# Kernel optimization log

Hardware: AMD Instinct MI355X
Metric: run time of the kernel (lower is better)

## Reference

```python
import jax, jax.numpy as jnp
import numpy as np

N = 50000
E = 800000
NFEAT = 256
NHID = 64
HEADS = 4
NCLASS = 16
NEG_SLOPE = 0.2


def setup_inputs() -> dict:
    key = jax.random.key(0)
    ks = jax.random.split(key, 12)
    g = lambda k, s, scale: (jax.random.normal(k, s, dtype=jnp.float32) * scale)
    inp = {
        "x": g(ks[0], (N, NFEAT), 1.0),
        "src": jax.random.randint(ks[1], (E,), 0, N, dtype=jnp.int32),
        "dst": jax.random.randint(ks[2], (E,), 0, N, dtype=jnp.int32),
        # layer 1 params (DGL GATConv: fc no-bias, attn_l/attn_r, output bias)
        "W1": g(ks[3], (NFEAT, HEADS * NHID), (2.0 / NFEAT) ** 0.5),
        "al1": g(ks[4], (HEADS, NHID), 0.1),
        "ar1": g(ks[5], (HEADS, NHID), 0.1),
        "b1": jnp.zeros((HEADS * NHID,), dtype=jnp.float32),
        # layer 2 params (1 head)
        "W2": g(ks[6], (HEADS * NHID, NCLASS), (2.0 / (HEADS * NHID)) ** 0.5),
        "al2": g(ks[7], (1, NCLASS), 0.1),
        "ar2": g(ks[8], (1, NCLASS), 0.1),
        "b2": jnp.zeros((NCLASS,), dtype=jnp.float32),
    }
    return inp


def gat_conv(x, src, dst, W, al, ar, b, heads, dh):
    # x: [N, Fin] -> feat: [N, H, D]
    n = x.shape[0]
    feat = (x @ W).reshape(n, heads, dh)
    el = jnp.einsum("nhd,hd->nh", feat, al)  # [N, H]
    er = jnp.einsum("nhd,hd->nh", feat, ar)
    e = jax.nn.leaky_relu(el[src] + er[dst], NEG_SLOPE)  # [E, H]
    # segment softmax over destination nodes
    emax = jax.ops.segment_max(e, dst, num_segments=n)
    emax = jnp.where(jnp.isfinite(emax), emax, jnp.float32(0.0))
    ex = jnp.exp(e - emax[dst])  # [E, H]
    denom = jax.ops.segment_sum(ex, dst, num_segments=n)  # [N, H]
    alpha = ex / denom[dst]  # [E, H]
    # gather src feats, weight, scatter-add to dst
    msg = feat[src] * alpha[:, :, None]  # [E, H, D]
    out = jax.ops.segment_sum(msg, dst, num_segments=n)  # [N, H, D]
    return out + b.reshape(1, heads, dh)


def reference(x, src, dst, W1, al1, ar1, b1, W2, al2, ar2, b2):
    h = gat_conv(x, src, dst, W1, al1, ar1, b1, HEADS, NHID)  # [N, 4, nhid]
    h = h.reshape(N, HEADS * NHID)
    h = jax.nn.elu(h)
    h = gat_conv(h, src, dst, W2, al2, ar2, b2, 1, NCLASS)  # [N, 1, nclass]
    h = h.reshape(N, NCLASS)
    return jax.nn.log_softmax(h, axis=1)
```

## Files before the change

kernel.cpp:

```cpp
#include <hip/hip_runtime.h>
#include <hip/hip_bf16.h>

#define N_NODES 50000
#define NP1     50001
#define N_EDGES 800000
#define NFEAT   256
#define NHID    64
#define HEADS   4
#define NCLASS  16
#define NEG_SLOPE 0.2f

#define NBLK  782
#define NBUCK 196
#define NSCAN (NBUCK * NBLK)
#define NSCB  150
#define MAXB  5120
#define NGB   391

typedef __attribute__((ext_vector_type(8))) short short8;
typedef __attribute__((ext_vector_type(4))) float floatx4;
typedef __attribute__((ext_vector_type(2))) float floatx2;

__device__ __forceinline__ float blo(unsigned int u) { return __uint_as_float(u << 16); }
__device__ __forceinline__ float bhi(unsigned int u) { return __uint_as_float(u & 0xffff0000u); }
__device__ __forceinline__ float b2f(unsigned short u) {
    return __uint_as_float(((unsigned int)u) << 16);
}
__device__ __forceinline__ unsigned short f2b(float f) {
    unsigned int x = __float_as_uint(f);
    unsigned int r = x + 0x7fffu + ((x >> 16) & 1u);
    return (unsigned short)(r >> 16);
}
__device__ __forceinline__ unsigned int pack2(float a, float b) {
    return (unsigned int)f2b(a) | ((unsigned int)f2b(b) << 16);
}
__device__ __forceinline__ float leaky(float x) { return fmaxf(x, NEG_SLOPE * x); }

__device__ __forceinline__ void fp8acc2(uint4 u, floatx2 exv, floatx2* acc) {
    acc[0] = __builtin_elementwise_fma(__builtin_amdgcn_cvt_pk_f32_fp8(u.x, 0), exv, acc[0]);
    acc[1] = __builtin_elementwise_fma(__builtin_amdgcn_cvt_pk_f32_fp8(u.x, 1), exv, acc[1]);
    acc[2] = __builtin_elementwise_fma(__builtin_amdgcn_cvt_pk_f32_fp8(u.y, 0), exv, acc[2]);
    acc[3] = __builtin_elementwise_fma(__builtin_amdgcn_cvt_pk_f32_fp8(u.y, 1), exv, acc[3]);
    acc[4] = __builtin_elementwise_fma(__builtin_amdgcn_cvt_pk_f32_fp8(u.z, 0), exv, acc[4]);
    acc[5] = __builtin_elementwise_fma(__builtin_amdgcn_cvt_pk_f32_fp8(u.z, 1), exv, acc[5]);
    acc[6] = __builtin_elementwise_fma(__builtin_amdgcn_cvt_pk_f32_fp8(u.w, 0), exv, acc[6]);
    acc[7] = __builtin_elementwise_fma(__builtin_amdgcn_cvt_pk_f32_fp8(u.w, 1), exv, acc[7]);
}

__global__ __launch_bounds__(256) void p1_kernel(
        const int* __restrict__ dst, int* __restrict__ bhist,
        const float* __restrict__ W1, const float* __restrict__ W2,
        const float* __restrict__ al1, const float* __restrict__ ar1,
        unsigned short* __restrict__ W1E, unsigned short* __restrict__ W2T) {
    __shared__ float tile[64][65];
    __shared__ int hist[NBUCK];
    int b = blockIdx.x, t = threadIdx.x;
    if (b < NBLK) {
        if (t < NBUCK) hist[t] = 0;
        __syncthreads();
        int e = (b * 256 + t) * 4;
        if (e < N_EDGES) {
            int4 d = *(const int4*)&dst[e];
            atomicAdd(&hist[d.x >> 8], 1);
            atomicAdd(&hist[d.y >> 8], 1);
            atomicAdd(&hist[d.z >> 8], 1);
            atomicAdd(&hist[d.w >> 8], 1);
        }
        __syncthreads();
        if (t < NBUCK) bhist[t * NBLK + b] = hist[t];
        return;
    }
    int pb = b - NBLK;
    if (pb < 16) {
        int tk = (pb & 3) * 64, tn = (pb >> 2) * 64;
        int tx = t & 63, ty = t >> 6;
#pragma unroll
        for (int r = 0; r < 16; ++r) {
            int row = ty * 16 + r;
            tile[row][tx] = W1[(tk + row) * 256 + tn + tx];
        }
        __syncthreads();
#pragma unroll
        for (int r = 0; r < 16; ++r) {
            int row = ty * 16 + r;
            W1E[(tn + row) * 256 + tk + tx] = f2b(tile[tx][row]);
        }
    } else if (pb < 20) {
        int h = pb - 16;
        int w = t >> 6, lane = t & 63;
        float alv = al1[h * 64 + lane];
        float arv = ar1[h * 64 + lane];
        for (int k = w; k < 256; k += 4) {
            float wv = W1[k * 256 + h * 64 + lane];
            float sl = wv * alv, sr = wv * arv;
#pragma unroll
            for (int off = 1; off < 64; off <<= 1) {
                sl += __shfl_xor(sl, off);
                sr += __shfl_xor(sr, off);
            }
            if (lane == 0) {
                W1E[(256 + h) * 256 + k] = f2b(sl);
                W1E[(260 + h) * 256 + k] = f2b(sr);
            }
        }
    } else {
        int n = t >> 4, k0 = (t & 15) * 16;
#pragma unroll
        for (int j = 0; j < 16; ++j)
            W2T[n * 256 + k0 + j] = f2b(W2[(k0 + j) * 16 + n]);
#pragma unroll
        for (int j = 0; j < 8; ++j)
            W1E[264 * 256 + j * 256 + t] = 0;
    }
}

__global__ __launch_bounds__(256) void scanA_kernel(const int* __restrict__ bhist,
                                                    int* __restrict__ partial,
                                                    int* __restrict__ bsum) {
    __shared__ int wsum[4];
    int t = threadIdx.x;
    int base = blockIdx.x * 1024 + t * 4;
    int v0 = (base + 0 < NSCAN) ? bhist[base + 0] : 0;
    int v1 = (base + 1 < NSCAN) ? bhist[base + 1] : 0;
    int v2 = (base + 2 < NSCAN) ? bhist[base + 2] : 0;
    int v3 = (base + 3 < NSCAN) ? bhist[base + 3] : 0;
    int s = v0 + v1 + v2 + v3;
    int lane = t & 63, w = t >> 6;
    int incl = s;
#pragma unroll
    for (int off = 1; off < 64; off <<= 1) {
        int x = __shfl_up(incl, off);
        if (lane >= off) incl += x;
    }
    if (lane == 63) wsum[w] = incl;
    __syncthreads();
    int woff = 0;
    for (int k = 0; k < w; ++k) woff += wsum[k];
    int excl = woff + incl - s;
    if (base + 0 < NSCAN) partial[base + 0] = excl;
    if (base + 1 < NSCAN) partial[base + 1] = excl + v0;
    if (base + 2 < NSCAN) partial[base + 2] = excl + v0 + v1;
    if (base + 3 < NSCAN) partial[base + 3] = excl + v0 + v1 + v2;
    if (t == 255) bsum[blockIdx.x] = woff + incl;
}

__global__ __launch_bounds__(256, 2) void p2g1_kernel(
        const int* __restrict__ src, const int* __restrict__ dst,
        const int* __restrict__ partial, const int* __restrict__ bsum,
        unsigned int* __restrict__ ebuf,
        const float* __restrict__ X, const unsigned short* __restrict__ BT,
        unsigned char* __restrict__ C, float* __restrict__ el, float* __restrict__ er) {
    __shared__ __align__(16) unsigned short As[128 * 40];
    __shared__ __align__(16) unsigned short Bs[272 * 40];
    __shared__ int wsum[4];
    __shared__ int sb[256];
    __shared__ int bs[NBUCK];
    __shared__ int lcnt[256];
    __shared__ int lofs[256];
    __shared__ int lfill[256];
    __shared__ unsigned int sorted[1024];

    int t = threadIdx.x;
    if (blockIdx.x >= NGB) {
        int b = blockIdx.x - NGB;
        int lane = t & 63, w = t >> 6;
        {
            int v = (t < NSCB) ? bsum[t] : 0;
            int incl = v;
#pragma unroll
            for (int off = 1; off < 64; off <<= 1) {
                int x = __shfl_up(incl, off);
                if (lane >= off) incl += x;
            }
            if (lane == 63) wsum[w] = incl;
            __syncthreads();
            int woff = 0;
            for (int k = 0; k < w; ++k) woff += wsum[k];
            sb[t] = woff + incl - v;
        }
        lcnt[t] = 0;
        __syncthreads();
        if (t < NBUCK) {
            int idx = t * NBLK + b;
            bs[t] = partial[idx] + sb[idx >> 10];
        }
        int e = (b * 256 + t) * 4;
        int4 d, s;
        bool valid = e < N_EDGES;
        if (valid) {
            d = *(const int4*)&dst[e];
            s = *(const int4*)&src[e];
            atomicAdd(&lcnt[d.x >> 8], 1);
            atomicAdd(&lcnt[d.y >> 8], 1);
            atomicAdd(&lcnt[d.z >> 8], 1);
            atomicAdd(&lcnt[d.w >> 8], 1);
        }
        __syncthreads();
        {
            int v = lcnt[t];
            int incl = v;
#pragma unroll
            for (int off = 1; off < 64; off <<= 1) {
                int x = __shfl_up(incl, off);
                if (lane >= off) incl += x;
            }
            if (lane == 63) wsum[w] = incl;
            __syncthreads();
            int woff = 0;
            for (int k = 0; k < w; ++k) woff += wsum[k];
            int excl = woff + incl - v;
            lofs[t] = excl;
            lfill[t] = excl;
        }
        __syncthreads();
        if (valid) {
            int p0 = atomicAdd(&lfill[d.x >> 8], 1);
            sorted[p0] = ((unsigned int)s.x << 16) | (unsigned int)d.x;
            int p1 = atomicAdd(&lfill[d.y >> 8], 1);
            sorted[p1] = ((unsigned int)s.y << 16) | (unsigned int)d.y;
            int p2 = atomicAdd(&lfill[d.z >> 8], 1);
            sorted[p2] = ((unsigned int)s.z << 16) | (unsigned int)d.z;
            int p3 = atomicAdd(&lfill[d.w >> 8], 1);
            sorted[p3] = ((unsigned int)s.w << 16) | (unsigned int)d.w;
        }
        __syncthreads();
        int ve = min(1024, N_EDGES - b * 1024);
        for (int i = t; i < ve; i += 256) {
            unsigned int p = sorted[i];
            int k = (p & 0xFFFFu) >> 8;
            ebuf[bs[k] + (i - lofs[k])] = p;
        }
        return;
    }

    int m0 = blockIdx.x * 128;
    int lane = t & 63, wm = t >> 6;
    int quad = lane >> 4, l16 = lane & 15;

    floatx4 acc[2][17];
#pragma unroll
    for (int i = 0; i < 2; ++i)
#pragma unroll
        for (int j = 0; j < 17; ++j) acc[i][j] = (floatx4){0.f, 0.f, 0.f, 0.f};

    int arow = t >> 1, ak = (t & 1) * 16;
    int grow = m0 + arow;
    const float* xrow = X + (size_t)grow * 256 + ak;

    for (int k0 = 0; k0 < 256; k0 += 32) {
        float4 v0 = make_float4(0.f, 0.f, 0.f, 0.f), v1 = v0, v2 = v0, v3 = v0;
        if (grow < N_NODES) {
            v0 = *(const float4*)(xrow + k0 + 0);
            v1 = *(const float4*)(xrow + k0 + 4);
            v2 = *(const float4*)(xrow + k0 + 8);
            v3 = *(const float4*)(xrow + k0 + 12);
        }
        uint4 p0, p1;
        p0.x = pack2(v0.x, v0.y); p0.y = pack2(v0.z, v0.w);
        p0.z = pack2(v1.x, v1.y); p0.w = pack2(v1.z, v1.w);
        p1.x = pack2(v2.x, v2.y); p1.y = pack2(v2.z, v2.w);
        p1.z = pack2(v3.x, v3.y); p1.w = pack2(v3.z, v3.w);
        *(uint4*)&As[arow * 40 + ak] = p0;
        *(uint4*)&As[arow * 40 + ak + 8] = p1;
#pragma unroll
        for (int i = 0; i < 5; ++i) {
            int ch = t + i * 256;
            if (ch < 1088) {
                int row = ch >> 2, off = (ch & 3) * 8;
                *(uint4*)&Bs[row * 40 + off] = *(const uint4*)(BT + row * 256 + k0 + off);
            }
        }
        __syncthreads();

        short8 a0 = *(const short8*)&As[(wm * 32 + l16) * 40 + quad * 8];
        short8 a1 = *(const short8*)&As[(wm * 32 + 16 + l16) * 40 + quad * 8];
#pragma unroll
        for (int nf = 0; nf < 17; ++nf) {
            short8 bb = *(const short8*)&Bs[(nf * 16 + l16) * 40 + quad * 8];
            acc[0][nf] = __builtin_amdgcn_mfma_f32_16x16x32_bf16(a0, bb, acc[0][nf], 0, 0, 0);
            acc[1][nf] = __builtin_amdgcn_mfma_f32_16x16x32_bf16(a1, bb, acc[1][nf], 0, 0, 0);
        }
        __syncthreads();
    }

#pragma unroll
    for (int mf = 0; mf < 2; ++mf) {
#pragma unroll
        for (int r = 0; r < 4; ++r) {
            int row = m0 + wm * 32 + mf * 16 + quad * 4 + r;
            if (row < N_NODES && l16 < 8) {
                float v = acc[mf][16][r];
                if (l16 < 4) el[row * 4 + l16] = v;
                else er[row * 4 + (l16 - 4)] = v;
            }
        }
    }

    unsigned short* scr = Bs + wm * 1536;
    int half = lane >> 5, l32 = lane & 31;
    int rrow = l32 >> 1, coff = (l32 & 1) * 8;
#pragma unroll
    for (int mf = 0; mf < 2; ++mf) {
#pragma unroll
        for (int p = 0; p < 8; ++p) {
            unsigned short* base = scr + (p & 1) * 768;
#pragma unroll
            for (int fr = 0; fr < 2; ++fr) {
                int nf = 2 * p + fr;
                unsigned short* fb = base + fr * 384;
#pragma unroll
                for (int r = 0; r < 4; ++r)
                    fb[(quad * 4 + r) * 24 + l16] = f2b(acc[mf][nf][r]);
            }
            uint4 val = *(const uint4*)(base + half * 384 + rrow * 24 + coff);
            int row = m0 + wm * 32 + mf * 16 + rrow;
            int nf = 2 * p + half;
            if (row < N_NODES) {
                float f0 = blo(val.x), f1 = bhi(val.x), f2 = blo(val.y), f3 = bhi(val.y);
                float f4 = blo(val.z), f5 = bhi(val.z), f6 = blo(val.w), f7 = bhi(val.w);
                int lo = __builtin_amdgcn_cvt_pk_fp8_f32(f0, f1, 0, 0);
                lo = __builtin_amdgcn_cvt_pk_fp8_f32(f2, f3, lo, 1);
                int hi = __builtin_amdgcn_cvt_pk_fp8_f32(f4, f5, 0, 0);
                hi = __builtin_amdgcn_cvt_pk_fp8_f32(f6, f7, hi, 1);
                uint2 o;
                o.x = (unsigned int)lo;
                o.y = (unsigned int)hi;
                *(uint2*)&C[(size_t)row * 256 + nf * 16 + coff] = o;
            }
        }
    }
}

__global__ __launch_bounds__(256) void p3_kernel(const int* __restrict__ partial,
                                                 const int* __restrict__ bsum,
                                                 const unsigned int* __restrict__ ebuf,
                                                 int* __restrict__ row_ptr,
                                                 int* __restrict__ csr_src) {
    __shared__ int wsum[4];
    __shared__ int sb[256];
    __shared__ int lcnt[256];
    __shared__ int lfill[256];
    __shared__ int sorted[MAXB];
    int b = blockIdx.x, t = threadIdx.x;
    int lane = t & 63, w = t >> 6;
    {
        int v = (t < NSCB) ? bsum[t] : 0;
        int incl = v;
#pragma unroll
        for (int off = 1; off < 64; off <<= 1) {
            int x = __shfl_up(incl, off);
            if (lane >= off) incl += x;
        }
        if (lane == 63) wsum[w] = incl;
        __syncthreads();
        int woff = 0;
        for (int k = 0; k < w; ++k) woff += wsum[k];
        sb[t] = woff + incl - v;
    }
    __syncthreads();
    int i0 = b * NBLK;
    int base = partial[i0] + sb[i0 >> 10];
    int endb;
    if (b == NBUCK - 1) endb = N_EDGES;
    else {
        int i1 = (b + 1) * NBLK;
        endb = partial[i1] + sb[i1 >> 10];
    }
    lcnt[t] = 0;
    __syncthreads();
    for (int i = base + t; i < endb; i += 256)
        atomicAdd(&lcnt[ebuf[i] & 255u], 1);
    __syncthreads();
    {
        int v = lcnt[t];
        int incl = v;
#pragma unroll
        for (int off = 1; off < 64; off <<= 1) {
            int x = __shfl_up(incl, off);
            if (lane >= off) incl += x;
        }
        if (lane == 63) wsum[w] = incl;
        __syncthreads();
        int woff = 0;
        for (int k = 0; k < w; ++k) woff += wsum[k];
        int excl = woff + incl - v;
        lfill[t] = excl;
        int node = b * 256 + t;
        if (node < NP1) row_ptr[node] = base + excl;
    }
    __syncthreads();
    for (int i = base + t; i < endb; i += 256) {
        unsigned int p = ebuf[i];
        int pos = atomicAdd(&lfill[p & 255u], 1);
        sorted[pos] = (int)(p >> 16);
    }
    __syncthreads();
    int M = endb - base;
    for (int i = t; i < M; i += 256)
        csr_src[base + i] = sorted[i];
}

__global__ void agg1_kernel(const unsigned char* __restrict__ feat1,
                            const float* __restrict__ el, const float* __restrict__ er,
                            const int* __restrict__ row_ptr, const int* __restrict__ csr_src,
                            const float* __restrict__ b1, unsigned short* __restrict__ h1b) {
    int wave = threadIdx.x >> 6, lane = threadIdx.x & 63;
    int n = blockIdx.x * 4 + wave;
    if (n >= N_NODES) return;
    int q = lane >> 4, l16 = lane & 15;
    int h = l16 >> 2;
    float er_h = er[n * 4 + h];
    int start = row_ptr[n], end = row_ptr[n + 1];

    floatx2 acc2[8];
#pragma unroll
    for (int j = 0; j < 8; ++j) acc2[j] = (floatx2){0.f, 0.f};
    float denom = 0.f;

    int i = start + q;
    for (; i + 4 < end; i += 8) {
        int s0 = csr_src[i];
        int s1 = csr_src[i + 4];
        float ex0 = __expf(leaky(el[s0 * 4 + h] + er_h));
        float ex1 = __expf(leaky(el[s1 * 4 + h] + er_h));
        uint4 a = *(const uint4*)(feat1 + (size_t)s0 * 256 + l16 * 16);
        uint4 b = *(const uint4*)(feat1 + (size_t)s1 * 256 + l16 * 16);
        denom += ex0 + ex1;
        fp8acc2(a, (floatx2){ex0, ex0}, acc2);
        fp8acc2(b, (floatx2){ex1, ex1}, acc2);
    }
    if (i < end) {
        int s = csr_src[i];
        float ex = __expf(leaky(el[s * 4 + h] + er_h));
        uint4 u = *(const uint4*)(feat1 + (size_t)s * 256 + l16 * 16);
        denom += ex;
        fp8acc2(u, (floatx2){ex, ex}, acc2);
    }
    float acc[16];
#pragma unroll
    for (int j = 0; j < 8; ++j) {
        acc[2 * j] = acc2[j][0];
        acc[2 * j + 1] = acc2[j][1];
    }
#pragma unroll
    for (int j = 0; j < 16; ++j) {
        acc[j] += __shfl_xor(acc[j], 16);
        acc[j] += __shfl_xor(acc[j], 32);
    }
    denom += __shfl_xor(denom, 16);
    denom += __shfl_xor(denom, 32);

    if (q == 0) {
        float inv = (end > start) ? 1.f / denom : 0.f;
        float o[16];
#pragma unroll
        for (int j = 0; j < 16; j += 4) {
            float4 b4 = *(const float4*)&b1[l16 * 16 + j];
            o[j + 0] = fmaf(acc[j + 0], inv, b4.x);
            o[j + 1] = fmaf(acc[j + 1], inv, b4.y);
            o[j + 2] = fmaf(acc[j + 2], inv, b4.z);
            o[j + 3] = fmaf(acc[j + 3], inv, b4.w);
        }
#pragma unroll
        for (int j = 0; j < 16; ++j) o[j] = o[j] > 0.f ? o[j] : __expf(o[j]) - 1.f;
        uint4 pa, pb;
        pa.x = pack2(o[0], o[1]);   pa.y = pack2(o[2], o[3]);
        pa.z = pack2(o[4], o[5]);   pa.w = pack2(o[6], o[7]);
        pb.x = pack2(o[8], o[9]);   pb.y = pack2(o[10], o[11]);
        pb.z = pack2(o[12], o[13]); pb.w = pack2(o[14], o[15]);
        uint4* dstp = (uint4*)(h1b + (size_t)n * 256 + l16 * 16);
        dstp[0] = pa;
        dstp[1] = pb;
    }
}

__global__ __launch_bounds__(256) void gemm2_mfma_kernel(
        const unsigned short* __restrict__ h1b, const unsigned short* __restrict__ W2T,
        const float* __restrict__ al2, const float* __restrict__ ar2,
        unsigned short* __restrict__ feat2b, float* __restrict__ el2, float* __restrict__ er2) {
    int wave = threadIdx.x >> 6, lane = threadIdx.x & 63;
    int l16 = lane & 15, quad = lane >> 4;
    int row0 = (blockIdx.x * 4 + wave) * 16;
    if (row0 >= N_NODES) return;
    floatx4 acc = (floatx4){0.f, 0.f, 0.f, 0.f};
    const unsigned short* arow = h1b + (size_t)(row0 + l16) * 256 + quad * 8;
    const unsigned short* brow = W2T + (size_t)l16 * 256 + quad * 8;
#pragma unroll
    for (int k0 = 0; k0 < 256; k0 += 32) {
        short8 a = *(const short8*)(arow + k0);
        short8 b = *(const short8*)(brow + k0);
        acc = __builtin_amdgcn_mfma_f32_16x16x32_bf16(a, b, acc, 0, 0, 0);
    }
    float a2 = al2[l16], r2 = ar2[l16];
#pragma unroll
    for (int r = 0; r < 4; ++r) {
        int row = row0 + quad * 4 + r;
        float v = acc[r];
        feat2b[row * 16 + l16] = f2b(v);
        float pl = v * a2, pr = v * r2;
#pragma unroll
        for (int off = 1; off < 16; off <<= 1) {
            pl += __shfl_xor(pl, off);
            pr += __shfl_xor(pr, off);
        }
        if (l16 == 0) {
            el2[row] = pl;
            er2[row] = pr;
        }
    }
}

__global__ void agg2_kernel(const unsigned short* __restrict__ feat2b,
                            const float* __restrict__ el2, const float* __restrict__ er2,
                            const int* __restrict__ row_ptr, const int* __restrict__ csr_src,
                            const float* __restrict__ b2, float* __restrict__ out) {
    int wave = threadIdx.x >> 6, lane = threadIdx.x & 63;
    int n = blockIdx.x * 4 + wave;
    if (n >= N_NODES) return;
    int start = row_ptr[n], end = row_ptr[n + 1];
    float ern = er2[n];
    int eo = lane >> 4, c = lane & 15;
    float acc = 0.f, denom = 0.f;
    int i = start + eo;
    for (; i + 4 < end; i += 8) {
        int s0 = csr_src[i], s1 = csr_src[i + 4];
        float ex0 = __expf(leaky(el2[s0] + ern));
        float ex1 = __expf(leaky(el2[s1] + ern));
        float f0 = b2f(feat2b[s0 * 16 + c]), f1 = b2f(feat2b[s1 * 16 + c]);
        denom += ex0 + ex1;
        acc = fmaf(f0, ex0, acc);
        acc = fmaf(f1, ex1, acc);
    }
    if (i < end) {
        int s = csr_src[i];
        float ex = __expf(leaky(el2[s] + ern));
        denom += ex;
        acc = fmaf(b2f(feat2b[s * 16 + c]), ex, acc);
    }
    acc += __shfl_xor(acc, 16);
    acc += __shfl_xor(acc, 32);
    denom += __shfl_xor(denom, 16);
    denom += __shfl_xor(denom, 32);
    float v = ((end > start) ? acc / denom : 0.f) + b2[c];
    float mx = v;
#pragma unroll
    for (int off = 1; off < 16; off <<= 1) mx = fmaxf(mx, __shfl_xor(mx, off));
    float ex2 = __expf(v - mx);
    float s2 = ex2;
#pragma unroll
    for (int off = 1; off < 16; off <<= 1) s2 += __shfl_xor(s2, off);
    float res = v - mx - logf(s2);
    if (lane < 16) out[n * 16 + lane] = res;
}

extern "C" void kernel_launch(void* const* d_in, const int* in_sizes, int n_in,
                              void* d_out, int out_size, void* d_ws, size_t ws_size,
                              hipStream_t stream) {
    const float* x   = (const float*)d_in[0];
    const int*   src = (const int*)d_in[1];
    const int*   dst = (const int*)d_in[2];
    const float* W1  = (const float*)d_in[3];
    const float* al1 = (const float*)d_in[4];
    const float* ar1 = (const float*)d_in[5];
    const float* b1  = (const float*)d_in[6];
    const float* W2  = (const float*)d_in[7];
    const float* al2 = (const float*)d_in[8];
    const float* ar2 = (const float*)d_in[9];
    const float* b2  = (const float*)d_in[10];
    float* out = (float*)d_out;

    char* ws = (char*)d_ws;
    size_t off = 0;
    auto alloc = [&](size_t bytes) -> void* {
        void* p = ws + off;
        off += (bytes + 255) & ~(size_t)255;
        return p;
    };
    unsigned short* W1E    = (unsigned short*)alloc((size_t)272 * 256 * 2);
    unsigned short* W2T    = (unsigned short*)alloc((size_t)16 * 256 * 2);
    unsigned char*  feat1  = (unsigned char*)alloc((size_t)N_NODES * 256);
    unsigned short* h1b    = (unsigned short*)alloc((size_t)N_NODES * 256 * 2);
    unsigned short* feat2b = (unsigned short*)alloc((size_t)N_NODES * 16 * 2);
    float* el1     = (float*)alloc((size_t)N_NODES * 4 * 4);
    float* er1     = (float*)alloc((size_t)N_NODES * 4 * 4);
    float* el2     = (float*)alloc((size_t)N_NODES * 4);
    float* er2     = (float*)alloc((size_t)N_NODES * 4);
    int*   bhist   = (int*)alloc((size_t)NSCAN * 4);
    int*   partial = (int*)alloc((size_t)NSCAN * 4);
    int*   bsum    = (int*)alloc((size_t)256 * 4);
    int*   row_ptr = (int*)alloc((size_t)NP1 * 4);
    unsigned int* ebuf = (unsigned int*)alloc((size_t)N_EDGES * 4);
    int*   csr_src = (int*)alloc((size_t)N_EDGES * 4);

    dim3 b256(256);
    p1_kernel<<<NBLK + 21, b256, 0, stream>>>(dst, bhist, W1, W2, al1, ar1, W1E, W2T);
    scanA_kernel<<<NSCB, b256, 0, stream>>>(bhist, partial, bsum);
    p2g1_kernel<<<NGB + NBLK, b256, 0, stream>>>(src, dst, partial, bsum, ebuf,
                                                 x, W1E, feat1, el1, er1);
    p3_kernel<<<NBUCK, b256, 0, stream>>>(partial, bsum, ebuf, row_ptr, csr_src);

    agg1_kernel<<<(N_NODES + 3) / 4, b256, 0, stream>>>(feat1, el1, er1, row_ptr, csr_src, b1, h1b);

    gemm2_mfma_kernel<<<(N_NODES + 63) / 64, b256, 0, stream>>>(h1b, W2T, al2, ar2, feat2b, el2, er2);
    agg2_kernel<<<(N_NODES + 3) / 4, b256, 0, stream>>>(feat2b, el2, er2, row_ptr, csr_src, b2, out);
}
```

Measured before the change: 245.0 us.

## Split layer-1 aggregation per head with head-major attention logits

The layer-1 aggregation kernel is reorganised so that each block handles one head for one half of the nodes, and each quarter-wave processes its own node. Blocks are ordered so that the eight head/half units run interleaved, which shrinks the working set of gathered source features per head to 64 bytes per node and aims to raise L2/MALL hit rates. The el/er logits are stored head-major (padded) so a head's logits are contiguous. In exchange, each source row is gathered four times in 64-byte pieces rather than once in 256 bytes, and there are more blocks and more row_ptr/csr_src reads.

```diff
diff --git a/kernel.cpp b/kernel.cpp
--- a/kernel.cpp
+++ b/kernel.cpp
@@ -16,6 +16,11 @@
 #define NSCB  150
 #define MAXB  5120
 #define NGB   391
+
+#define ELP    50048
+#define HALF_N 25000
+#define AGG1_BPU 1563
+#define AGG1_NB  (8 * AGG1_BPU)
 
 typedef __attribute__((ext_vector_type(8))) short short8;
 typedef __attribute__((ext_vector_type(4))) float floatx4;
@@ -290,8 +295,8 @@
             int row = m0 + wm * 32 + mf * 16 + quad * 4 + r;
             if (row < N_NODES && l16 < 8) {
                 float v = acc[mf][16][r];
-                if (l16 < 4) el[row * 4 + l16] = v;
-                else er[row * 4 + (l16 - 4)] = v;
+                if (l16 < 4) el[l16 * ELP + row] = v;
+                else er[(l16 - 4) * ELP + row] = v;
             }
         }
     }
@@ -400,42 +405,56 @@
         csr_src[base + i] = sorted[i];
 }
 
-__global__ void agg1_kernel(const unsigned char* __restrict__ feat1,
-                            const float* __restrict__ el, const float* __restrict__ er,
-                            const int* __restrict__ row_ptr, const int* __restrict__ csr_src,
-                            const float* __restrict__ b1, unsigned short* __restrict__ h1b) {
+__global__ __launch_bounds__(256) void agg1_kernel(
+        const unsigned char* __restrict__ feat1,
+        const float* __restrict__ el, const float* __restrict__ er,
+        const int* __restrict__ row_ptr, const int* __restrict__ csr_src,
+        const float* __restrict__ b1, unsigned short* __restrict__ h1b) {
+    int b = blockIdx.x;
+    int unit = b & 7;
+    int chunk = b >> 3;
+    int head = unit >> 1;
+    int half = unit & 1;
     int wave = threadIdx.x >> 6, lane = threadIdx.x & 63;
-    int n = blockIdx.x * 4 + wave;
-    if (n >= N_NODES) return;
-    int q = lane >> 4, l16 = lane & 15;
-    int h = l16 >> 2;
-    float er_h = er[n * 4 + h];
-    int start = row_ptr[n], end = row_ptr[n + 1];
+    int quad = lane >> 4, l16 = lane & 15;
+    int slot = l16 >> 2, l4 = l16 & 3;
+    int nloc = chunk * 16 + wave * 4 + quad;
+    bool vn = nloc < HALF_N;
+    int n = half * HALF_N + nloc;
+    int start = 0, end = 0;
+    if (vn) {
+        start = row_ptr[n];
+        end = row_ptr[n + 1];
+    }
+    float er_h = vn ? er[head * ELP + n] : 0.f;
+    const float* elh = el + head * ELP;
+    const unsigned char* fbase = feat1 + head * 64 + l4 * 16;
 
     floatx2 acc2[8];
 #pragma unroll
     for (int j = 0; j < 8; ++j) acc2[j] = (floatx2){0.f, 0.f};
     float denom = 0.f;
 
-    int i = start + q;
+    int i = start + slot;
     for (; i + 4 < end; i += 8) {
         int s0 = csr_src[i];
         int s1 = csr_src[i + 4];
-        float ex0 = __expf(leaky(el[s0 * 4 + h] + er_h));
-        float ex1 = __expf(leaky(el[s1 * 4 + h] + er_h));
-        uint4 a = *(const uint4*)(feat1 + (size_t)s0 * 256 + l16 * 16);
-        uint4 b = *(const uint4*)(feat1 + (size_t)s1 * 256 + l16 * 16);
+        float ex0 = __expf(leaky(elh[s0] + er_h));
+        float ex1 = __expf(leaky(elh[s1] + er_h));
+        uint4 a = *(const uint4*)(fbase + (size_t)s0 * 256);
+        uint4 c = *(const uint4*)(fbase + (size_t)s1 * 256);
         denom += ex0 + ex1;
         fp8acc2(a, (floatx2){ex0, ex0}, acc2);
-        fp8acc2(b, (floatx2){ex1, ex1}, acc2);
+        fp8acc2(c, (floatx2){ex1, ex1}, acc2);
     }
     if (i < end) {
         int s = csr_src[i];
-        float ex = __expf(leaky(el[s * 4 + h] + er_h));
-        uint4 u = *(const uint4*)(feat1 + (size_t)s * 256 + l16 * 16);
+        float ex = __expf(leaky(elh[s] + er_h));
+        uint4 u = *(const uint4*)(fbase + (size_t)s * 256);
         denom += ex;
         fp8acc2(u, (floatx2){ex, ex}, acc2);
     }
+
     float acc[16];
 #pragma unroll
     for (int j = 0; j < 8; ++j) {
@@ -444,33 +463,34 @@
     }
 #pragma unroll
     for (int j = 0; j < 16; ++j) {
-        acc[j] += __shfl_xor(acc[j], 16);
-        acc[j] += __shfl_xor(acc[j], 32);
-    }
-    denom += __shfl_xor(denom, 16);
-    denom += __shfl_xor(denom, 32);
-
-    if (q == 0) {
-        float inv = (end > start) ? 1.f / denom : 0.f;
-        float o[16];
-#pragma unroll
-        for (int j = 0; j < 16; j += 4) {
-            float4 b4 = *(const float4*)&b1[l16 * 16 + j];
-            o[j + 0] = fmaf(acc[j + 0], inv, b4.x);
-            o[j + 1] = fmaf(acc[j + 1], inv, b4.y);
-            o[j + 2] = fmaf(acc[j + 2], inv, b4.z);
-            o[j + 3] = fmaf(acc[j + 3], inv, b4.w);
-        }
-#pragma unroll
-        for (int j = 0; j < 16; ++j) o[j] = o[j] > 0.f ? o[j] : __expf(o[j]) - 1.f;
-        uint4 pa, pb;
-        pa.x = pack2(o[0], o[1]);   pa.y = pack2(o[2], o[3]);
-        pa.z = pack2(o[4], o[5]);   pa.w = pack2(o[6], o[7]);
-        pb.x = pack2(o[8], o[9]);   pb.y = pack2(o[10], o[11]);
-        pb.z = pack2(o[12], o[13]); pb.w = pack2(o[14], o[15]);
-        uint4* dstp = (uint4*)(h1b + (size_t)n * 256 + l16 * 16);
-        dstp[0] = pa;
-        dstp[1] = pb;
+        acc[j] += __shfl_xor(acc[j], 4);
+        acc[j] += __shfl_xor(acc[j], 8);
+    }
+    denom += __shfl_xor(denom, 4);
+    denom += __shfl_xor(denom, 8);
+
+    float inv = (end > start) ? 1.f / denom : 0.f;
+    bool sb0 = slot & 1, sb1 = slot & 2;
+    float o[4];
+#pragma unroll
+    for (int k = 0; k < 4; ++k) {
+        float tA = sb1 ? acc[8 + k] : acc[k];
+        float tB = sb1 ? acc[12 + k] : acc[4 + k];
+        o[k] = sb0 ? tB : tA;
+    }
+    int fo = l4 * 16 + slot * 4;
+    float4 b4 = *(const float4*)&b1[head * 64 + fo];
+    o[0] = fmaf(o[0], inv, b4.x);
+    o[1] = fmaf(o[1], inv, b4.y);
+    o[2] = fmaf(o[2], inv, b4.z);
+    o[3] = fmaf(o[3], inv, b4.w);
+#pragma unroll
+    for (int k = 0; k < 4; ++k) o[k] = o[k] > 0.f ? o[k] : __expf(o[k]) - 1.f;
+    if (vn) {
+        uint2 p;
+        p.x = pack2(o[0], o[1]);
+        p.y = pack2(o[2], o[3]);
+        *(uint2*)&h1b[(size_t)n * 256 + head * 64 + fo] = p;
     }
 }
 
@@ -581,8 +601,8 @@
     unsigned char*  feat1  = (unsigned char*)alloc((size_t)N_NODES * 256);
     unsigned short* h1b    = (unsigned short*)alloc((size_t)N_NODES * 256 * 2);
     unsigned short* feat2b = (unsigned short*)alloc((size_t)N_NODES * 16 * 2);
-    float* el1     = (float*)alloc((size_t)N_NODES * 4 * 4);
-    float* er1     = (float*)alloc((size_t)N_NODES * 4 * 4);
+    float* el1     = (float*)alloc((size_t)4 * ELP * 4);
+    float* er1     = (float*)alloc((size_t)4 * ELP * 4);
     float* el2     = (float*)alloc((size_t)N_NODES * 4);
     float* er2     = (float*)alloc((size_t)N_NODES * 4);
     int*   bhist   = (int*)alloc((size_t)NSCAN * 4);
@@ -599,7 +619,7 @@
                                                  x, W1E, feat1, el1, er1);
     p3_kernel<<<NBUCK, b256, 0, stream>>>(partial, bsum, ebuf, row_ptr, csr_src);
 
-    agg1_kernel<<<(N_NODES + 3) / 4, b256, 0, stream>>>(feat1, el1, er1, row_ptr, csr_src, b1, h1b);
+    agg1_kernel<<<AGG1_NB, b256, 0, stream>>>(feat1, el1, er1, row_ptr, csr_src, b1, h1b);
 
     gemm2_mfma_kernel<<<(N_NODES + 63) / 64, b256, 0, stream>>>(h1b, W2T, al2, ar2, feat2b, el2, er2);
     agg2_kernel<<<(N_NODES + 3) / 4, b256, 0, stream>>>(feat2b, el2, er2, row_ptr, csr_src, b2, out);
```

New measurement: 270.5 us. 1.1x slower.

## Precompute per-edge attention exponentials in separate kernels and spread agg1 output writes

Applied to the files above, without the earlier changes.

Splits the per-edge exp(leaky(el+er)) computation out of both aggregation kernels into new exk1/exk2 kernels that write per-edge weights to workspace arrays. In layer 1 this removes redundant exponentials, since each of 4 lanes per head previously recomputed the same value. The aggregation kernels then read the precomputed weights, trading compute for extra global traffic (about 16 MB written and read for ex1) plus two more kernel launches. The agg1 epilogue now has all four quads each write a quarter of the output row instead of quad 0 writing the whole row.

```diff
diff --git a/kernel.cpp b/kernel.cpp
--- a/kernel.cpp
+++ b/kernel.cpp
@@ -400,16 +400,46 @@
         csr_src[base + i] = sorted[i];
 }
 
-__global__ void agg1_kernel(const unsigned char* __restrict__ feat1,
-                            const float* __restrict__ el, const float* __restrict__ er,
-                            const int* __restrict__ row_ptr, const int* __restrict__ csr_src,
-                            const float* __restrict__ b1, unsigned short* __restrict__ h1b) {
+__global__ __launch_bounds__(256) void exk1_kernel(
+        const float* __restrict__ el, const float* __restrict__ er,
+        const int* __restrict__ row_ptr, const int* __restrict__ csr_src,
+        float* __restrict__ ex1) {
+    int wave = threadIdx.x >> 6, lane = threadIdx.x & 63;
+    int n = blockIdx.x * 4 + wave;
+    if (n >= N_NODES) return;
+    int e16 = lane >> 2, h = lane & 3;
+    float er_h = er[n * 4 + h];
+    int start = row_ptr[n], end = row_ptr[n + 1];
+    for (int i = start + e16; i < end; i += 16) {
+        int s = csr_src[i];
+        ex1[(size_t)i * 4 + h] = __expf(leaky(el[s * 4 + h] + er_h));
+    }
+}
+
+__global__ __launch_bounds__(256) void exk2_kernel(
+        const float* __restrict__ el2, const float* __restrict__ er2,
+        const int* __restrict__ row_ptr, const int* __restrict__ csr_src,
+        float* __restrict__ ex2) {
+    int wave = threadIdx.x >> 6, lane = threadIdx.x & 63;
+    int n = blockIdx.x * 4 + wave;
+    if (n >= N_NODES) return;
+    float ern = er2[n];
+    int start = row_ptr[n], end = row_ptr[n + 1];
+    for (int i = start + lane; i < end; i += 64) {
+        int s = csr_src[i];
+        ex2[i] = __expf(leaky(el2[s] + ern));
+    }
+}
+
+__global__ __launch_bounds__(256) void agg1_kernel(
+        const unsigned char* __restrict__ feat1, const float* __restrict__ ex1,
+        const int* __restrict__ row_ptr, const int* __restrict__ csr_src,
+        const float* __restrict__ b1, unsigned short* __restrict__ h1b) {
     int wave = threadIdx.x >> 6, lane = threadIdx.x & 63;
     int n = blockIdx.x * 4 + wave;
     if (n >= N_NODES) return;
     int q = lane >> 4, l16 = lane & 15;
     int h = l16 >> 2;
-    float er_h = er[n * 4 + h];
     int start = row_ptr[n], end = row_ptr[n + 1];
 
     floatx2 acc2[8];
@@ -421,20 +451,20 @@
     for (; i + 4 < end; i += 8) {
         int s0 = csr_src[i];
         int s1 = csr_src[i + 4];
-        float ex0 = __expf(leaky(el[s0 * 4 + h] + er_h));
-        float ex1 = __expf(leaky(el[s1 * 4 + h] + er_h));
+        float e0 = ex1[(size_t)i * 4 + h];
+        float e1 = ex1[(size_t)(i + 4) * 4 + h];
         uint4 a = *(const uint4*)(feat1 + (size_t)s0 * 256 + l16 * 16);
         uint4 b = *(const uint4*)(feat1 + (size_t)s1 * 256 + l16 * 16);
-        denom += ex0 + ex1;
-        fp8acc2(a, (floatx2){ex0, ex0}, acc2);
-        fp8acc2(b, (floatx2){ex1, ex1}, acc2);
+        denom += e0 + e1;
+        fp8acc2(a, (floatx2){e0, e0}, acc2);
+        fp8acc2(b, (floatx2){e1, e1}, acc2);
     }
     if (i < end) {
         int s = csr_src[i];
-        float ex = __expf(leaky(el[s * 4 + h] + er_h));
+        float e = ex1[(size_t)i * 4 + h];
         uint4 u = *(const uint4*)(feat1 + (size_t)s * 256 + l16 * 16);
-        denom += ex;
-        fp8acc2(u, (floatx2){ex, ex}, acc2);
+        denom += e;
+        fp8acc2(u, (floatx2){e, e}, acc2);
     }
     float acc[16];
 #pragma unroll
@@ -450,28 +480,26 @@
     denom += __shfl_xor(denom, 16);
     denom += __shfl_xor(denom, 32);
 
-    if (q == 0) {
-        float inv = (end > start) ? 1.f / denom : 0.f;
-        float o[16];
-#pragma unroll
-        for (int j = 0; j < 16; j += 4) {
-            float4 b4 = *(const float4*)&b1[l16 * 16 + j];
-            o[j + 0] = fmaf(acc[j + 0], inv, b4.x);
-            o[j + 1] = fmaf(acc[j + 1], inv, b4.y);
-            o[j + 2] = fmaf(acc[j + 2], inv, b4.z);
-            o[j + 3] = fmaf(acc[j + 3], inv, b4.w);
-        }
-#pragma unroll
-        for (int j = 0; j < 16; ++j) o[j] = o[j] > 0.f ? o[j] : __expf(o[j]) - 1.f;
-        uint4 pa, pb;
-        pa.x = pack2(o[0], o[1]);   pa.y = pack2(o[2], o[3]);
-        pa.z = pack2(o[4], o[5]);   pa.w = pack2(o[6], o[7]);
-        pb.x = pack2(o[8], o[9]);   pb.y = pack2(o[10], o[11]);
-        pb.z = pack2(o[12], o[13]); pb.w = pack2(o[14], o[15]);
-        uint4* dstp = (uint4*)(h1b + (size_t)n * 256 + l16 * 16);
-        dstp[0] = pa;
-        dstp[1] = pb;
-    }
+    float inv = (end > start) ? 1.f / denom : 0.f;
+    bool qb0 = q & 1, qb1 = q & 2;
+    float o[4];
+#pragma unroll
+    for (int k = 0; k < 4; ++k) {
+        float tA = qb1 ? acc[8 + k] : acc[k];
+        float tB = qb1 ? acc[12 + k] : acc[4 + k];
+        o[k] = qb0 ? tB : tA;
+    }
+    float4 b4 = *(const float4*)&b1[l16 * 16 + q * 4];
+    o[0] = fmaf(o[0], inv, b4.x);
+    o[1] = fmaf(o[1], inv, b4.y);
+    o[2] = fmaf(o[2], inv, b4.z);
+    o[3] = fmaf(o[3], inv, b4.w);
+#pragma unroll
+    for (int k = 0; k < 4; ++k) o[k] = o[k] > 0.f ? o[k] : __expf(o[k]) - 1.f;
+    uint2 p;
+    p.x = pack2(o[0], o[1]);
+    p.y = pack2(o[2], o[3]);
+    *(uint2*)&h1b[(size_t)n * 256 + l16 * 16 + q * 4] = p;
 }
 
 __global__ __launch_bounds__(256) void gemm2_mfma_kernel(
@@ -510,32 +538,30 @@
     }
 }
 
-__global__ void agg2_kernel(const unsigned short* __restrict__ feat2b,
-                            const float* __restrict__ el2, const float* __restrict__ er2,
-                            const int* __restrict__ row_ptr, const int* __restrict__ csr_src,
-                            const float* __restrict__ b2, float* __restrict__ out) {
+__global__ __launch_bounds__(256) void agg2_kernel(
+        const unsigned short* __restrict__ feat2b, const float* __restrict__ ex2,
+        const int* __restrict__ row_ptr, const int* __restrict__ csr_src,
+        const float* __restrict__ b2, float* __restrict__ out) {
     int wave = threadIdx.x >> 6, lane = threadIdx.x & 63;
     int n = blockIdx.x * 4 + wave;
     if (n >= N_NODES) return;
     int start = row_ptr[n], end = row_ptr[n + 1];
-    float ern = er2[n];
     int eo = lane >> 4, c = lane & 15;
     float acc = 0.f, denom = 0.f;
     int i = start + eo;
     for (; i + 4 < end; i += 8) {
         int s0 = csr_src[i], s1 = csr_src[i + 4];
-        float ex0 = __expf(leaky(el2[s0] + ern));
-        float ex1 = __expf(leaky(el2[s1] + ern));
+        float e0 = ex2[i], e1 = ex2[i + 4];
         float f0 = b2f(feat2b[s0 * 16 + c]), f1 = b2f(feat2b[s1 * 16 + c]);
-        denom += ex0 + ex1;
-        acc = fmaf(f0, ex0, acc);
-        acc = fmaf(f1, ex1, acc);
+        denom += e0 + e1;
+        acc = fmaf(f0, e0, acc);
+        acc = fmaf(f1, e1, acc);
     }
     if (i < end) {
         int s = csr_src[i];
-        float ex = __expf(leaky(el2[s] + ern));
-        denom += ex;
-        acc = fmaf(b2f(feat2b[s * 16 + c]), ex, acc);
+        float e = ex2[i];
+        denom += e;
+        acc = fmaf(b2f(feat2b[s * 16 + c]), e, acc);
     }
     acc += __shfl_xor(acc, 16);
     acc += __shfl_xor(acc, 32);
@@ -545,8 +571,8 @@
     float mx = v;
 #pragma unroll
     for (int off = 1; off < 16; off <<= 1) mx = fmaxf(mx, __shfl_xor(mx, off));
-    float ex2 = __expf(v - mx);
-    float s2 = ex2;
+    float ex = __expf(v - mx);
+    float s2 = ex;
 #pragma unroll
     for (int off = 1; off < 16; off <<= 1) s2 += __shfl_xor(s2, off);
     float res = v - mx - logf(s2);
@@ -591,6 +617,8 @@
     int*   row_ptr = (int*)alloc((size_t)NP1 * 4);
     unsigned int* ebuf = (unsigned int*)alloc((size_t)N_EDGES * 4);
     int*   csr_src = (int*)alloc((size_t)N_EDGES * 4);
+    float* ex1     = (float*)alloc((size_t)N_EDGES * 4 * 4);
+    float* ex2     = (float*)alloc((size_t)N_EDGES * 4);
 
     dim3 b256(256);
     p1_kernel<<<NBLK + 21, b256, 0, stream>>>(dst, bhist, W1, W2, al1, ar1, W1E, W2T);
@@ -599,8 +627,10 @@
                                                  x, W1E, feat1, el1, er1);
     p3_kernel<<<NBUCK, b256, 0, stream>>>(partial, bsum, ebuf, row_ptr, csr_src);
 
-    agg1_kernel<<<(N_NODES + 3) / 4, b256, 0, stream>>>(feat1, el1, er1, row_ptr, csr_src, b1, h1b);
+    exk1_kernel<<<(N_NODES + 3) / 4, b256, 0, stream>>>(el1, er1, row_ptr, csr_src, ex1);
+    agg1_kernel<<<(N_NODES + 3) / 4, b256, 0, stream>>>(feat1, ex1, row_ptr, csr_src, b1, h1b);
 
     gemm2_mfma_kernel<<<(N_NODES + 63) / 64, b256, 0, stream>>>(h1b, W2T, al2, ar2, feat2b, el2, er2);
-    agg2_kernel<<<(N_NODES + 3) / 4, b256, 0, stream>>>(feat2b, el2, er2, row_ptr, csr_src, b2, out);
-}
+    exk2_kernel<<<(N_NODES + 3) / 4, b256, 0, stream>>>(el2, er2, row_ptr, csr_src, ex2);
+    agg2_kernel<<<(N_NODES + 3) / 4, b256, 0, stream>>>(feat2b, ex2, row_ptr, csr_src, b2, out);
+}
```

After: 281.5 us. +14.9%, slower.

## Assign one destination node per 16-lane group in layer-1 aggregation

Applied to the files above, without the earlier changes.

The layer-1 aggregation kernel previously split each node's edges across four 16-lane quarters of a wave and combined them with cross-lane shuffles. Now each quarter handles a separate node and walks that node's whole edge list, so the shuffle reduction goes away and a quarter of the blocks are launched. The cost is divergence inside a wave when the four nodes have different degrees, and a longer serial edge loop per node.

```diff
diff --git a/kernel.cpp b/kernel.cpp
--- a/kernel.cpp
+++ b/kernel.cpp
@@ -405,73 +405,68 @@
                             const int* __restrict__ row_ptr, const int* __restrict__ csr_src,
                             const float* __restrict__ b1, unsigned short* __restrict__ h1b) {
     int wave = threadIdx.x >> 6, lane = threadIdx.x & 63;
-    int n = blockIdx.x * 4 + wave;
-    if (n >= N_NODES) return;
     int q = lane >> 4, l16 = lane & 15;
+    int n = (blockIdx.x * 4 + wave) * 4 + q;
+    bool vn = n < N_NODES;
     int h = l16 >> 2;
-    float er_h = er[n * 4 + h];
-    int start = row_ptr[n], end = row_ptr[n + 1];
+    int start = 0, end = 0;
+    if (vn) {
+        start = row_ptr[n];
+        end = row_ptr[n + 1];
+    }
+    float er_h = vn ? er[n * 4 + h] : 0.f;
 
     floatx2 acc2[8];
 #pragma unroll
     for (int j = 0; j < 8; ++j) acc2[j] = (floatx2){0.f, 0.f};
     float denom = 0.f;
 
-    int i = start + q;
-    for (; i + 4 < end; i += 8) {
+    int i = start;
+    for (; i + 1 < end; i += 2) {
         int s0 = csr_src[i];
-        int s1 = csr_src[i + 4];
-        float ex0 = __expf(leaky(el[s0 * 4 + h] + er_h));
-        float ex1 = __expf(leaky(el[s1 * 4 + h] + er_h));
+        int s1 = csr_src[i + 1];
+        float e0 = __expf(leaky(el[s0 * 4 + h] + er_h));
+        float e1 = __expf(leaky(el[s1 * 4 + h] + er_h));
         uint4 a = *(const uint4*)(feat1 + (size_t)s0 * 256 + l16 * 16);
         uint4 b = *(const uint4*)(feat1 + (size_t)s1 * 256 + l16 * 16);
-        denom += ex0 + ex1;
-        fp8acc2(a, (floatx2){ex0, ex0}, acc2);
-        fp8acc2(b, (floatx2){ex1, ex1}, acc2);
+        denom += e0 + e1;
+        fp8acc2(a, (floatx2){e0, e0}, acc2);
+        fp8acc2(b, (floatx2){e1, e1}, acc2);
     }
     if (i < end) {
         int s = csr_src[i];
-        float ex = __expf(leaky(el[s * 4 + h] + er_h));
+        float e = __expf(leaky(el[s * 4 + h] + er_h));
         uint4 u = *(const uint4*)(feat1 + (size_t)s * 256 + l16 * 16);
-        denom += ex;
-        fp8acc2(u, (floatx2){ex, ex}, acc2);
-    }
-    float acc[16];
+        denom += e;
+        fp8acc2(u, (floatx2){e, e}, acc2);
+    }
+    if (!vn) return;
+
+    float inv = (end > start) ? 1.f / denom : 0.f;
+    float o[16];
 #pragma unroll
     for (int j = 0; j < 8; ++j) {
-        acc[2 * j] = acc2[j][0];
-        acc[2 * j + 1] = acc2[j][1];
-    }
-#pragma unroll
-    for (int j = 0; j < 16; ++j) {
-        acc[j] += __shfl_xor(acc[j], 16);
-        acc[j] += __shfl_xor(acc[j], 32);
-    }
-    denom += __shfl_xor(denom, 16);
-    denom += __shfl_xor(denom, 32);
-
-    if (q == 0) {
-        float inv = (end > start) ? 1.f / denom : 0.f;
-        float o[16];
-#pragma unroll
-        for (int j = 0; j < 16; j += 4) {
-            float4 b4 = *(const float4*)&b1[l16 * 16 + j];
-            o[j + 0] = fmaf(acc[j + 0], inv, b4.x);
-            o[j + 1] = fmaf(acc[j + 1], inv, b4.y);
-            o[j + 2] = fmaf(acc[j + 2], inv, b4.z);
-            o[j + 3] = fmaf(acc[j + 3], inv, b4.w);
-        }
-#pragma unroll
-        for (int j = 0; j < 16; ++j) o[j] = o[j] > 0.f ? o[j] : __expf(o[j]) - 1.f;
-        uint4 pa, pb;
-        pa.x = pack2(o[0], o[1]);   pa.y = pack2(o[2], o[3]);
-        pa.z = pack2(o[4], o[5]);   pa.w = pack2(o[6], o[7]);
-        pb.x = pack2(o[8], o[9]);   pb.y = pack2(o[10], o[11]);
-        pb.z = pack2(o[12], o[13]); pb.w = pack2(o[14], o[15]);
-        uint4* dstp = (uint4*)(h1b + (size_t)n * 256 + l16 * 16);
-        dstp[0] = pa;
-        dstp[1] = pb;
-    }
+        o[2 * j] = acc2[j][0];
+        o[2 * j + 1] = acc2[j][1];
+    }
+#pragma unroll
+    for (int j = 0; j < 16; j += 4) {
+        float4 b4 = *(const float4*)&b1[l16 * 16 + j];
+        o[j + 0] = fmaf(o[j + 0], inv, b4.x);
+        o[j + 1] = fmaf(o[j + 1], inv, b4.y);
+        o[j + 2] = fmaf(o[j + 2], inv, b4.z);
+        o[j + 3] = fmaf(o[j + 3], inv, b4.w);
+    }
+#pragma unroll
+    for (int j = 0; j < 16; ++j) o[j] = o[j] > 0.f ? o[j] : __expf(o[j]) - 1.f;
+    uint4 pa, pb;
+    pa.x = pack2(o[0], o[1]);   pa.y = pack2(o[2], o[3]);
+    pa.z = pack2(o[4], o[5]);   pa.w = pack2(o[6], o[7]);
+    pb.x = pack2(o[8], o[9]);   pb.y = pack2(o[10], o[11]);
+    pb.z = pack2(o[12], o[13]); pb.w = pack2(o[14], o[15]);
+    uint4* dstp = (uint4*)(h1b + (size_t)n * 256 + l16 * 16);
+    dstp[0] = pa;
+    dstp[1] = pb;
 }
 
 __global__ __launch_bounds__(256) void gemm2_mfma_kernel(
@@ -599,7 +594,7 @@
                                                  x, W1E, feat1, el1, er1);
     p3_kernel<<<NBUCK, b256, 0, stream>>>(partial, bsum, ebuf, row_ptr, csr_src);
 
-    agg1_kernel<<<(N_NODES + 3) / 4, b256, 0, stream>>>(feat1, el1, er1, row_ptr, csr_src, b1, h1b);
+    agg1_kernel<<<(N_NODES + 15) / 16, b256, 0, stream>>>(feat1, el1, er1, row_ptr, csr_src, b1, h1b);
 
     gemm2_mfma_kernel<<<(N_NODES + 63) / 64, b256, 0, stream>>>(h1b, W2T, al2, ar2, feat2b, el2, er2);
     agg2_kernel<<<(N_NODES + 3) / 4, b256, 0, stream>>>(feat2b, el2, er2, row_ptr, csr_src, b2, out);
```

Measured after the change: 242.5 us. No clear change (-1.0%).
